# Performance work log

Hardware: AMD Instinct MI355X
Metric: run time of the kernel (lower is better)

Reference implementation:

```python
import jax, jax.numpy as jnp
import numpy as np

N = 100000       # nodes
E = 1600000      # edges (avg degree 16)
F_IN = 64        # node feature dim
H = 8            # GAT heads
C1 = 8           # gat1 out_channels per head (8*8=64)
C2 = 10          # gat2 out_channels = num classes
S = 32           # edge_feats sequence length
SMAX = 32        # s_max padding target
DM = 6           # transformer d_model (SelfAttention dim_out default)
NH = 2           # transformer heads
DIN = 10         # transformer dim_in
NEG = 0.2        # leaky relu negative slope
EPS = 1e-5       # LayerNorm eps


def setup_inputs() -> dict:
    key = jax.random.key(0)
    ks = jax.random.split(key, 32)
    rn = lambda k, shp, s=0.1: jax.random.normal(k, shp, jnp.float32) * s
    inp = {
        'x': jax.random.normal(ks[0], (N, F_IN), jnp.float32),
        'edge_index': jax.random.randint(ks[1], (2, E), 0, N, jnp.int32),
        'edge_feats': jax.random.normal(ks[2], (N, S, DIN), jnp.float32),
        # gat1: weight [in, heads*out], att [1, H, 2*C1], bias [H*C1]
        'W1': rn(ks[3], (F_IN, H * C1)), 'att1': rn(ks[4], (1, H, 2 * C1)), 'b1': jnp.zeros((H * C1,), jnp.float32),
        # gat2: in=70 (64 gat1 + 6 transformer), concat=False -> bias [C2]
        'W2': rn(ks[5], (70, H * C2)), 'att2': rn(ks[6], (1, H, 2 * C2)), 'b2': jnp.zeros((C2,), jnp.float32),
        # transformer Encoder (weights stored [in, out])
        'Wq': rn(ks[7], (DIN, DM)), 'bq': rn(ks[8], (DM,)),
        'Wk': rn(ks[9], (DIN, DM)), 'bk': rn(ks[10], (DM,)),
        'Wv': rn(ks[11], (DIN, DM)), 'bv': rn(ks[12], (DM,)),
        'g0': jnp.ones((DM,), jnp.float32), 'be0': jnp.zeros((DM,), jnp.float32),
        'Wf1': rn(ks[13], (DM, 4 * DM)), 'bf1': rn(ks[14], (4 * DM,)),
        'Wf2': rn(ks[15], (4 * DM, DM)), 'bf2': rn(ks[16], (DM,)),
        'g1': jnp.ones((DM,), jnp.float32), 'be1': jnp.zeros((DM,), jnp.float32),
        'Wrep': rn(ks[17], (SMAX, 1)), 'brep': rn(ks[18], (1,)),
    }
    return inp


def _layer_norm(x, g, b):
    m = x.mean(-1, keepdims=True)
    v = ((x - m) ** 2).mean(-1, keepdims=True)
    return (x - m) / jnp.sqrt(v + EPS) * g + b


def _gat_conv(x, src, dst, W, att, bias, heads, outc, concat):
    """GATConv: remove self loops (masking), add one self loop per node,
    edge-wise attention, per-destination segment softmax, scatter-add."""
    n = x.shape[0]
    valid = src != dst                       # remove_self_loops (mask, static shape)
    loop = jnp.arange(n, dtype=src.dtype)    # add_self_loops
    s = jnp.concatenate([src, loop])
    d = jnp.concatenate([dst, loop])
    valid = jnp.concatenate([valid, jnp.ones((n,), bool)])
    xw = (x @ W).reshape(n, heads, outc)     # [N, H, C]
    xj = xw[s]                               # gather source feats  [E', H, C]
    xi = xw[d]                               # gather target feats  [E', H, C]
    a_i, a_j = att[0, :, :outc], att[0, :, outc:]
    alpha = (xi * a_i).sum(-1) + (xj * a_j).sum(-1)          # [E', H]
    alpha = jnp.where(alpha >= 0, alpha, NEG * alpha)         # leaky relu
    alpha = jnp.where(valid[:, None], alpha, -jnp.inf)        # drop input self-loops
    amax = jax.ops.segment_max(alpha, d, num_segments=n)      # segment softmax
    ea = jnp.exp(alpha - amax[d])
    denom = jax.ops.segment_sum(ea, d, num_segments=n)
    w = ea / denom[d]
    out = jax.ops.segment_sum(xj * w[:, :, None], d, num_segments=n)  # [N, H, C]
    if concat:
        return out.reshape(n, heads * outc) + bias
    return out.mean(axis=1) + bias


def _encoder(Xf, Wq, bq, Wk, bk, Wv, bv, g0, be0, Wf1, bf1, Wf2, bf2, g1, be1, Wrep, brep):
    n, s, _ = Xf.shape
    Q = Xf @ Wq + bq
    K = Xf @ Wk + bk
    V = Xf @ Wv + bv
    dh = DM // NH
    Qh = Q.reshape(n, s, NH, dh).transpose(0, 2, 1, 3)   # [n, h, s, dh]
    Kh = K.reshape(n, s, NH, dh).transpose(0, 2, 1, 3)
    Vh = V.reshape(n, s, NH, dh).transpose(0, 2, 1, 3)
    scale = 1.0 / np.float32(np.sqrt(DM))                # note: sqrt(d_model), as in source
    A = jax.nn.softmax(jnp.einsum('nhsd,nhtd->nhst', Qh, Kh) * scale, axis=-1)
    A1 = jnp.einsum('nhst,nhtd->nhsd', A, Vh)
    O = (Qh + A1).transpose(0, 2, 1, 3).reshape(n, s, DM)  # skip=True path
    O = _layer_norm(O, g0, be0)
    ff = jnp.maximum(O @ Wf1 + bf1, 0.0) @ Wf2 + bf2
    O = _layer_norm(O + ff, g1, be1)
    O = O.transpose(0, 2, 1)                              # [n, DM, s]
    O = jnp.pad(O, ((0, 0), (0, 0), (0, SMAX - s)))
    O = O @ Wrep + brep                                   # fc_rep: [n, DM, 1]
    return O[..., 0]                                      # squeeze -> [n, DM]


def reference(x, edge_index, edge_feats, W1, att1, b1, W2, att2, b2,
              Wq, bq, Wk, bk, Wv, bv, g0, be0, Wf1, bf1, Wf2, bf2,
              g1, be1, Wrep, brep):
    src, dst = edge_index[0], edge_index[1]
    h1 = _gat_conv(x, src, dst, W1, att1, b1, H, C1, True)          # [N, 64]
    h1 = jax.nn.elu(h1)
    xt = _encoder(edge_feats, Wq, bq, Wk, bk, Wv, bv, g0, be0,
                  Wf1, bf1, Wf2, bf2, g1, be1, Wrep, brep)          # [N, 6]
    h2 = _gat_conv(jnp.concatenate([h1, xt], axis=1), src, dst,
                   W2, att2, b2, H, C2, False)                      # [N, 10]
    return jax.nn.log_softmax(h2, axis=1)
```

## Files before the change

kernel.cpp:

```cpp
#include <hip/hip_runtime.h>
#include <hip/hip_bf16.h>


#define NEG_SLOPE 0.2f

using short8  = __attribute__((ext_vector_type(8))) short;
using floatx4 = __attribute__((ext_vector_type(4))) float;

__device__ __forceinline__ float bf_lo(unsigned u) { return __uint_as_float(u << 16); }
__device__ __forceinline__ float bf_hi(unsigned u) { return __uint_as_float(u & 0xffff0000u); }
__device__ __forceinline__ unsigned pk(float lo, float hi)
{
    __hip_bfloat16 l = __float2bfloat16(lo), h = __float2bfloat16(hi);
    unsigned ul = reinterpret_cast<unsigned short&>(l);
    unsigned uh = reinterpret_cast<unsigned short&>(h);
    return ul | (uh << 16);
}
__device__ __forceinline__ short bfs(float f)
{
    __hip_bfloat16 b = __float2bfloat16(f);
    return reinterpret_cast<short&>(b);
}

__global__ void __launch_bounds__(256) front_kernel(
    const float* __restrict__ Xf,
    const float* __restrict__ Wq, const float* __restrict__ bq,
    const float* __restrict__ Wk, const float* __restrict__ bk,
    const float* __restrict__ Wv, const float* __restrict__ bv,
    const float* __restrict__ g0, const float* __restrict__ be0,
    const float* __restrict__ Wf1, const float* __restrict__ bf1,
    const float* __restrict__ Wf2, const float* __restrict__ bf2,
    const float* __restrict__ g1, const float* __restrict__ be1,
    const float* __restrict__ Wrep, const float* __restrict__ brep,
    __hip_bfloat16* __restrict__ hx,
    const int* __restrict__ src, const int* __restrict__ dst,
    int* __restrict__ deg, int* __restrict__ rank, int e,
    int n, int EB)
{
    __shared__ float smem[3072];
    int t = threadIdx.x;
    int bid = blockIdx.x;

    if (bid < EB) {
        float* sh = smem;
        size_t base = (size_t)bid * 2560;
#pragma unroll
        for (int i = 0; i < 10; ++i) sh[i * 256 + t] = Xf[base + i * 256 + t];
        __syncthreads();

        int sub = t >> 5;
        int s   = t & 31;
        int v   = bid * 8 + sub;

        float xv[10];
#pragma unroll
        for (int i = 0; i < 10; ++i) xv[i] = sh[sub * 320 + s * 10 + i];
        __syncthreads();

        float q[6], k[6], w[6];
#pragma unroll
        for (int j = 0; j < 6; ++j) { q[j] = bq[j]; k[j] = bk[j]; w[j] = bv[j]; }
#pragma unroll
        for (int i = 0; i < 10; ++i) {
#pragma unroll
            for (int j = 0; j < 6; ++j) {
                q[j] += xv[i] * Wq[i * 6 + j];
                k[j] += xv[i] * Wk[i * 6 + j];
                w[j] += xv[i] * Wv[i * 6 + j];
            }
        }

        float* kv = sh + sub * 384;
        *(float4*)&kv[s * 12 + 0] = make_float4(k[0], k[1], k[2], k[3]);
        *(float4*)&kv[s * 12 + 4] = make_float4(k[4], k[5], w[0], w[1]);
        *(float4*)&kv[s * 12 + 8] = make_float4(w[2], w[3], w[4], w[5]);
        __builtin_amdgcn_wave_barrier();

        const float scale = 0.40824829046386301637f;
        float q0s = q[0] * scale, q1s = q[1] * scale, q2s = q[2] * scale;
        float q3s = q[3] * scale, q4s = q[4] * scale, q5s = q[5] * scale;

        float dA0 = 0.f, dB0 = 0.f, dA1 = 0.f, dB1 = 0.f;
        float aA00 = 0.f, aA01 = 0.f, aA02 = 0.f;
        float aB00 = 0.f, aB01 = 0.f, aB02 = 0.f;
        float aA10 = 0.f, aA11 = 0.f, aA12 = 0.f;
        float aB10 = 0.f, aB11 = 0.f, aB12 = 0.f;

#pragma unroll 4
        for (int t2 = 0; t2 < 32; t2 += 2) {
            float4 A0 = *(const float4*)&kv[t2 * 12 + 0];
            float4 A1 = *(const float4*)&kv[t2 * 12 + 4];
            float4 A2 = *(const float4*)&kv[t2 * 12 + 8];
            float4 B0 = *(const float4*)&kv[t2 * 12 + 12];
            float4 B1 = *(const float4*)&kv[t2 * 12 + 16];
            float4 B2 = *(const float4*)&kv[t2 * 12 + 20];
            {
                float p0 = __expf(q0s * A0.x + q1s * A0.y + q2s * A0.z);
                float p1 = __expf(q3s * A0.w + q4s * A1.x + q5s * A1.y);
                dA0 += p0; aA00 += p0 * A1.z; aA01 += p0 * A1.w; aA02 += p0 * A2.x;
                dA1 += p1; aA10 += p1 * A2.y; aA11 += p1 * A2.z; aA12 += p1 * A2.w;
            }
            {
                float p0 = __expf(q0s * B0.x + q1s * B0.y + q2s * B0.z);
                float p1 = __expf(q3s * B0.w + q4s * B1.x + q5s * B1.y);
                dB0 += p0; aB00 += p0 * B1.z; aB01 += p0 * B1.w; aB02 += p0 * B2.x;
                dB1 += p1; aB10 += p1 * B2.y; aB11 += p1 * B2.z; aB12 += p1 * B2.w;
            }
        }

        float O[6];
        {
            float inv0 = 1.f / (dA0 + dB0);
            float inv1 = 1.f / (dA1 + dB1);
            O[0] = q[0] + (aA00 + aB00) * inv0;
            O[1] = q[1] + (aA01 + aB01) * inv0;
            O[2] = q[2] + (aA02 + aB02) * inv0;
            O[3] = q[3] + (aA10 + aB10) * inv1;
            O[4] = q[4] + (aA11 + aB11) * inv1;
            O[5] = q[5] + (aA12 + aB12) * inv1;
        }

        {
            float mean = (O[0] + O[1] + O[2] + O[3] + O[4] + O[5]) * (1.f / 6.f);
            float var = 0.f;
#pragma unroll
            for (int j = 0; j < 6; ++j) { float d = O[j] - mean; var += d * d; }
            var *= (1.f / 6.f);
            float r = rsqrtf(var + 1e-5f);
#pragma unroll
            for (int j = 0; j < 6; ++j) O[j] = (O[j] - mean) * r * g0[j] + be0[j];
        }

        float f[6];
#pragma unroll
        for (int j = 0; j < 6; ++j) f[j] = O[j] + bf2[j];
#pragma unroll 4
        for (int r = 0; r < 24; ++r) {
            float hr = bf1[r];
#pragma unroll
            for (int j = 0; j < 6; ++j) hr += O[j] * Wf1[j * 24 + r];
            hr = fmaxf(hr, 0.f);
#pragma unroll
            for (int j = 0; j < 6; ++j) f[j] += hr * Wf2[r * 6 + j];
        }
        {
            float mean = (f[0] + f[1] + f[2] + f[3] + f[4] + f[5]) * (1.f / 6.f);
            float var = 0.f;
#pragma unroll
            for (int j = 0; j < 6; ++j) { float d = f[j] - mean; var += d * d; }
            var *= (1.f / 6.f);
            float r = rsqrtf(var + 1e-5f);
#pragma unroll
            for (int j = 0; j < 6; ++j) f[j] = (f[j] - mean) * r * g1[j] + be1[j];
        }

        float wr = Wrep[s];
#pragma unroll
        for (int j = 0; j < 6; ++j) {
            float val = f[j] * wr;
#pragma unroll
            for (int off = 16; off >= 1; off >>= 1) val += __shfl_xor(val, off, 32);
            f[j] = val;
        }
        if (s == 0) {
            float br = brep[0];
#pragma unroll
            for (int j = 0; j < 6; ++j)
                hx[(size_t)v * 96 + 64 + j] = __float2bfloat16(f[j] + br);
        }
    } else {
        int i = (bid - EB) * 256 + t;
        if (i < e) {
            int ss = src[i], dd = dst[i];
            if (ss != dd) rank[i] = atomicAdd(&deg[dd], 1);
        }
    }
}

__global__ void __launch_bounds__(256) w1ext_kernel(
    const float* __restrict__ W1, const float* __restrict__ att1,
    __hip_bfloat16* __restrict__ w1t)
{
    int idx = blockIdx.x * 256 + threadIdx.x;
    if (idx >= 80 * 64) return;
    int j = idx / 64, k = idx % 64;
    float val;
    if (j < 64) {
        val = W1[k * 64 + j];
    } else if (j < 72) {
        int h = j - 64;
        val = 0.f;
        for (int c = 0; c < 8; ++c)
            val += W1[k * 64 + h * 8 + c] * att1[h * 16 + c];
    } else {
        int h = j - 72;
        val = 0.f;
        for (int c = 0; c < 8; ++c)
            val += W1[k * 64 + h * 8 + c] * att1[h * 16 + 8 + c];
    }
    w1t[j * 64 + k] = __float2bfloat16(val);
}

__global__ void __launch_bounds__(256) xw1mfma_kernel(
    const float* __restrict__ x, const __hip_bfloat16* __restrict__ w1t,
    __hip_bfloat16* __restrict__ xwb, float* __restrict__ ai,
    unsigned* __restrict__ ajp, int n)
{
    int t = threadIdx.x, wv = t >> 6, l = t & 63;
    int base = blockIdx.x * 64 + wv * 16;
    if (base >= n) return;

    int mrow = l & 15;
    int kc   = (l >> 4) * 8;
    int dr0  = (l >> 4) * 4;

    const float* xr = x + (size_t)(base + mrow) * 64;
    short8 a0, a1;
#pragma unroll
    for (int i = 0; i < 8; ++i) {
        a0[i] = bfs(xr[kc + i]);
        a1[i] = bfs(xr[32 + kc + i]);
    }

    const short* wp = (const short*)w1t;

#pragma unroll
    for (int nt = 0; nt < 5; ++nt) {
        int col = nt * 16 + mrow;
        short8 b0 = *(const short8*)(wp + (size_t)col * 64 + kc);
        short8 b1 = *(const short8*)(wp + (size_t)col * 64 + 32 + kc);
        floatx4 acc = {0.f, 0.f, 0.f, 0.f};
        acc = __builtin_amdgcn_mfma_f32_16x16x32_bf16(a0, b0, acc, 0, 0, 0);
        acc = __builtin_amdgcn_mfma_f32_16x16x32_bf16(a1, b1, acc, 0, 0, 0);
        if (nt < 4) {
#pragma unroll
            for (int r = 0; r < 4; ++r) {
                int m = base + dr0 + r;
                xwb[(size_t)m * 64 + nt * 16 + mrow] = __float2bfloat16(acc[r]);
            }
        } else {
#pragma unroll
            for (int r = 0; r < 4; ++r) {
                int m = base + dr0 + r;
                float val = acc[r];
                float nb  = __shfl_xor(val, 1, 64);
                if (mrow < 8) {
                    ai[(size_t)m * 8 + mrow] = val;
                } else {
                    int h = mrow - 8;
                    if ((h & 1) == 0)
                        ajp[(size_t)m * 4 + (h >> 1)] = pk(val, nb);
                }
            }
        }
    }
}

__global__ void __launch_bounds__(1024) scan1_kernel(
    const int* __restrict__ deg, int* __restrict__ bsum, int n)
{
    __shared__ int sh[1024];
    int t = threadIdx.x;
    int i = blockIdx.x * 1024 + t;
    sh[t] = (i < n) ? deg[i] : 0;
    __syncthreads();
    for (int off = 512; off >= 1; off >>= 1) {
        if (t < off) sh[t] += sh[t + off];
        __syncthreads();
    }
    if (t == 0) bsum[blockIdx.x] = sh[0];
}

__global__ void __launch_bounds__(128) scan2_kernel(int* __restrict__ bsum, int nb)
{
    __shared__ int sh[128];
    int t = threadIdx.x;
    int v = (t < nb) ? bsum[t] : 0;
    sh[t] = v;
    __syncthreads();
    for (int off = 1; off < 128; off <<= 1) {
        int val = (t >= off) ? sh[t - off] : 0;
        __syncthreads();
        sh[t] += val;
        __syncthreads();
    }
    if (t < nb) bsum[t] = sh[t] - v;
}

__global__ void __launch_bounds__(1024) scan3_kernel(
    const int* __restrict__ deg, const int* __restrict__ bsum,
    int* __restrict__ offs, int n)
{
    __shared__ int sh[1024];
    int t = threadIdx.x;
    int i = blockIdx.x * 1024 + t;
    int v = (i < n) ? deg[i] : 0;
    sh[t] = v;
    __syncthreads();
    for (int off = 1; off < 1024; off <<= 1) {
        int val = (t >= off) ? sh[t - off] : 0;
        __syncthreads();
        sh[t] += val;
        __syncthreads();
    }
    if (i < n) offs[i] = bsum[blockIdx.x] + sh[t] - v;
}

__global__ void scatter_kernel(const int* __restrict__ src, const int* __restrict__ dst,
                               const int* __restrict__ offsets,
                               const int* __restrict__ rank,
                               int* __restrict__ elist, int e)
{
    int i = blockIdx.x * blockDim.x + threadIdx.x;
    if (i < e) {
        int s = src[i], d = dst[i];
        if (s != d) elist[offsets[d] + rank[i]] = s;
    }
}

__global__ void __launch_bounds__(256) agg1_kernel(
    const __hip_bfloat16* __restrict__ xwb, const float* __restrict__ ai1,
    const unsigned* __restrict__ ajp, const float* __restrict__ att1,
    const float* __restrict__ b1,
    const int* __restrict__ offs, const int* __restrict__ deg,
    const int* __restrict__ elist,
    __hip_bfloat16* __restrict__ hx, int n)
{
    int t = threadIdx.x, wv = t >> 6, l = t & 63;
    int v = blockIdx.x * 4 + wv;
    int h = l >> 3, c = l & 7;
    int e1 = l >> 3, hp = l & 7;

    float ai_l = ai1[(size_t)v * 8 + h];
    float ai_p = ai1[(size_t)v * 8 + hp];
    float attj_l = att1[h * 16 + 8 + c];

    float yself = __bfloat162float(xwb[(size_t)v * 64 + l]);
    float ps = yself * attj_l;
    ps += __shfl_xor(ps, 1, 64);
    ps += __shfl_xor(ps, 2, 64);
    ps += __shfl_xor(ps, 4, 64);
    float a = ai_l + ps;
    a = fmaxf(a, NEG_SLOPE * a);
    float ea  = __expf(a);
    float acc = ea * yself;

    float den_acc = 0.f;
    int off = offs[v], dg = deg[v];
    for (int j = 0; j < dg; j += 8) {
        int idxv = 0;
        if (l < 8 && j + l < dg) idxv = elist[off + j + l];
        int se = __shfl(idxv, e1, 64);
        unsigned aw = ajp[(size_t)se * 4 + (hp >> 1)];
        float ajv = (hp & 1) ? bf_hi(aw) : bf_lo(aw);
        float u = ai_p + ajv;
        u = fmaxf(u, NEG_SLOPE * u);
        float wl = __expf(u);
        wl = (j + e1 < dg) ? wl : 0.f;
        den_acc += wl;
#pragma unroll
        for (int b = 0; b < 8; ++b) {
            int s = __shfl(idxv, b, 64);
            float y = __bfloat162float(xwb[(size_t)s * 64 + l]);
            float w = __shfl(wl, b * 8 + h, 64);
            acc += w * y;
        }
    }
    den_acc += __shfl_xor(den_acc, 8, 64);
    den_acc += __shfl_xor(den_acc, 16, 64);
    den_acc += __shfl_xor(den_acc, 32, 64);
    float den = ea + __shfl(den_acc, h, 64);

    float o = acc / den + b1[l];
    o = o > 0.f ? o : expm1f(o);
    hx[(size_t)v * 96 + l] = __float2bfloat16(o);
}

__global__ void __launch_bounds__(256) w2ext_kernel(
    const float* __restrict__ W2, const float* __restrict__ att2,
    __hip_bfloat16* __restrict__ w2t)
{
    int idx = blockIdx.x * 256 + threadIdx.x;
    if (idx >= 96 * 96) return;
    int j = idx / 96, k = idx % 96;
    float val = 0.f;
    if (k < 70) {
        if (j < 80) {
            val = W2[k * 80 + j];
        } else if (j < 88) {
            int h = j - 80;
            for (int c = 0; c < 10; ++c)
                val += W2[k * 80 + h * 10 + c] * att2[h * 20 + c];
        } else {
            int h = j - 88;
            for (int c = 0; c < 10; ++c)
                val += W2[k * 80 + h * 10 + c] * att2[h * 20 + 10 + c];
        }
    }
    w2t[j * 96 + k] = __float2bfloat16(val);
}

__global__ void __launch_bounds__(256) xw2mfma_kernel(
    const __hip_bfloat16* __restrict__ hx, const __hip_bfloat16* __restrict__ w2t,
    __hip_bfloat16* __restrict__ xw2p, float* __restrict__ ai2, int n)
{
    int t = threadIdx.x, wv = t >> 6, l = t & 63;
    int base = blockIdx.x * 64 + wv * 16;
    if (base >= n) return;

    int mrow = l & 15;
    int kc   = (l >> 4) * 8;
    int dr0  = (l >> 4) * 4;

    const short* hp = (const short*)hx;
    const short* wp = (const short*)w2t;

    short8 a0 = *(const short8*)(hp + (size_t)(base + mrow) * 96 + 0  + kc);
    short8 a1 = *(const short8*)(hp + (size_t)(base + mrow) * 96 + 32 + kc);
    short8 a2 = *(const short8*)(hp + (size_t)(base + mrow) * 96 + 64 + kc);

#pragma unroll
    for (int nt = 0; nt < 6; ++nt) {
        int col = nt * 16 + mrow;
        short8 b0 = *(const short8*)(wp + (size_t)col * 96 + 0  + kc);
        short8 b1 = *(const short8*)(wp + (size_t)col * 96 + 32 + kc);
        short8 b2 = *(const short8*)(wp + (size_t)col * 96 + 64 + kc);
        floatx4 acc = {0.f, 0.f, 0.f, 0.f};
        acc = __builtin_amdgcn_mfma_f32_16x16x32_bf16(a0, b0, acc, 0, 0, 0);
        acc = __builtin_amdgcn_mfma_f32_16x16x32_bf16(a1, b1, acc, 0, 0, 0);
        acc = __builtin_amdgcn_mfma_f32_16x16x32_bf16(a2, b2, acc, 0, 0, 0);
#pragma unroll
        for (int r = 0; r < 4; ++r) {
            int m = base + dr0 + r;
            float val = acc[r];
            if (nt < 5) {
                xw2p[(size_t)m * 128 + nt * 16 + mrow] = __float2bfloat16(val);
            } else {
                if (mrow < 8) ai2[(size_t)m * 8 + mrow] = val;
                else xw2p[(size_t)m * 128 + 80 + (mrow - 8)] = __float2bfloat16(val);
            }
        }
    }
}

__global__ void __launch_bounds__(256) agg2_kernel(
    const unsigned* __restrict__ xw2p, const float* __restrict__ ai2,
    const float* __restrict__ b2,
    const int* __restrict__ offs, const int* __restrict__ deg,
    const int* __restrict__ elist, float* __restrict__ out, int n)
{
    __shared__ float buf[4][80];
    __shared__ float buf2[4][10];
    int t = threadIdx.x, wv = t >> 6, l = t & 63;
    int v = blockIdx.x * 4 + wv;

    int hc = (l < 40) ? (l / 5) : 0;
    int e1 = l >> 3, hp = l & 7;
    float ai_p = ai2[(size_t)v * 8 + hp];
    float ai_l = (l < 40) ? ai2[(size_t)v * 8 + hc] : 0.f;

    bool act = l < 44;
    unsigned selfw = act ? xw2p[(size_t)v * 64 + l] : 0u;
    int ajl = 40 + (hc >> 1);
    unsigned ajw = __shfl(selfw, ajl, 64);
    float ajs = (hc & 1) ? bf_hi(ajw) : bf_lo(ajw);
    float a = ai_l + ajs;
    a = fmaxf(a, NEG_SLOPE * a);
    float e0 = __expf(a);
    float acc0 = e0 * bf_lo(selfw), acc1 = e0 * bf_hi(selfw);

    float den_acc = 0.f;
    int off = offs[v], dg = deg[v];
    for (int j = 0; j < dg; j += 8) {
        int idxv = 0;
        if (l < 8 && j + l < dg) idxv = elist[off + j + l];
        int se = __shfl(idxv, e1, 64);
        unsigned aw = xw2p[(size_t)se * 64 + 40 + (hp >> 1)];
        float ajv = (hp & 1) ? bf_hi(aw) : bf_lo(aw);
        float u = ai_p + ajv;
        u = fmaxf(u, NEG_SLOPE * u);
        float wl = __expf(u);
        wl = (j + e1 < dg) ? wl : 0.f;
        den_acc += wl;
#pragma unroll
        for (int b = 0; b < 8; ++b) {
            int s = __shfl(idxv, b, 64);
            unsigned yw = (l < 40) ? xw2p[(size_t)s * 64 + l] : 0u;
            float w = __shfl(wl, b * 8 + hc, 64);
            acc0 += w * bf_lo(yw);
            acc1 += w * bf_hi(yw);
        }
    }
    den_acc += __shfl_xor(den_acc, 8, 64);
    den_acc += __shfl_xor(den_acc, 16, 64);
    den_acc += __shfl_xor(den_acc, 32, 64);
    float den = e0 + __shfl(den_acc, hc, 64);

    if (l < 40) {
        float inv = 1.f / den;
        buf[wv][2 * l]     = acc0 * inv;
        buf[wv][2 * l + 1] = acc1 * inv;
    }
    __builtin_amdgcn_wave_barrier();
    if (l < 10) {
        float mval = 0.f;
#pragma unroll
        for (int hh = 0; hh < 8; ++hh) mval += buf[wv][hh * 10 + l];
        buf2[wv][l] = mval * 0.125f + b2[l];
    }
    __builtin_amdgcn_wave_barrier();
    if (l < 10) {
        float mx = -1e30f;
#pragma unroll
        for (int cc = 0; cc < 10; ++cc) mx = fmaxf(mx, buf2[wv][cc]);
        float se = 0.f;
#pragma unroll
        for (int cc = 0; cc < 10; ++cc) se += __expf(buf2[wv][cc] - mx);
        out[(size_t)v * 10 + l] = buf2[wv][l] - mx - __logf(se);
    }
}

extern "C" void kernel_launch(void* const* d_in, const int* in_sizes, int n_in,
                              void* d_out, int out_size, void* d_ws, size_t ws_size,
                              hipStream_t stream)
{
    const float* x    = (const float*)d_in[0];
    const int*   ei   = (const int*)  d_in[1];
    const float* ef   = (const float*)d_in[2];
    const float* W1   = (const float*)d_in[3];
    const float* att1 = (const float*)d_in[4];
    const float* b1   = (const float*)d_in[5];
    const float* W2   = (const float*)d_in[6];
    const float* att2 = (const float*)d_in[7];
    const float* b2   = (const float*)d_in[8];
    const float* Wq   = (const float*)d_in[9];
    const float* bq   = (const float*)d_in[10];
    const float* Wk   = (const float*)d_in[11];
    const float* bk   = (const float*)d_in[12];
    const float* Wv   = (const float*)d_in[13];
    const float* bv   = (const float*)d_in[14];
    const float* g0   = (const float*)d_in[15];
    const float* be0  = (const float*)d_in[16];
    const float* Wf1  = (const float*)d_in[17];
    const float* bf1  = (const float*)d_in[18];
    const float* Wf2  = (const float*)d_in[19];
    const float* bf2  = (const float*)d_in[20];
    const float* g1   = (const float*)d_in[21];
    const float* be1  = (const float*)d_in[22];
    const float* Wrep = (const float*)d_in[23];
    const float* brep = (const float*)d_in[24];

    const int n = in_sizes[0] / 64;
    const int e = in_sizes[1] / 2;
    const int* src = ei;
    const int* dst = ei + e;

    char* ws = (char*)d_ws;
    size_t o = 0;
    auto alloc = [&](size_t bytes) -> void* {
        void* p = ws + o;
        o += (bytes + 255) & ~(size_t)255;
        return p;
    };
    __hip_bfloat16* xw1b = (__hip_bfloat16*)alloc((size_t)n * 64 * 2);
    __hip_bfloat16* hx   = (__hip_bfloat16*)alloc((size_t)n * 96 * 2);
    __hip_bfloat16* xw2p = (__hip_bfloat16*)alloc((size_t)n * 128 * 2);
    __hip_bfloat16* w2t  = (__hip_bfloat16*)alloc(96 * 96 * 2);
    __hip_bfloat16* w1t  = (__hip_bfloat16*)alloc(80 * 64 * 2);
    unsigned* ajp = (unsigned*)alloc((size_t)n * 4 * 4);
    float* ai1   = (float*)alloc((size_t)n * 8 * 4);
    float* ai2   = (float*)alloc((size_t)n * 8 * 4);
    int*   deg   = (int*)  alloc((size_t)n * 4);
    int*   offs  = (int*)  alloc((size_t)n * 4);
    int*   rank  = (int*)  alloc((size_t)e * 4);
    int*   bsum  = (int*)  alloc(256 * 4);
    int*   elist = (int*)  alloc((size_t)e * 4);
    (void)ws_size; (void)n_in; (void)out_size;

    hipMemsetAsync(deg, 0, (size_t)n * 4, stream);
    hipMemsetAsync(hx, 0, (size_t)n * 96 * 2, stream);

    const int NB = (n + 1023) / 1024;
    const int EB = n / 8;
    const int CB = (e + 255) / 256;

    w2ext_kernel<<<36, 256, 0, stream>>>(W2, att2, w2t);
    w1ext_kernel<<<20, 256, 0, stream>>>(W1, att1, w1t);
    front_kernel<<<EB + CB, 256, 0, stream>>>(
        ef, Wq, bq, Wk, bk, Wv, bv, g0, be0, Wf1, bf1, Wf2, bf2, g1, be1,
        Wrep, brep, hx,
        src, dst, deg, rank, e,
        n, EB);
    xw1mfma_kernel<<<(n + 63) / 64, 256, 0, stream>>>(x, w1t, xw1b, ai1, ajp, n);
    scan1_kernel<<<NB, 1024, 0, stream>>>(deg, bsum, n);
    scan2_kernel<<<1, 128, 0, stream>>>(bsum, NB);
    scan3_kernel<<<NB, 1024, 0, stream>>>(deg, bsum, offs, n);
    scatter_kernel<<<(e + 255) / 256, 256, 0, stream>>>(src, dst, offs, rank,
                                                        elist, e);
    agg1_kernel<<<n / 4, 256, 0, stream>>>(xw1b, ai1, ajp, att1, b1,
                                           offs, deg, elist, hx, n);
    xw2mfma_kernel<<<(n + 63) / 64, 256, 0, stream>>>(hx, w2t, xw2p, ai2, n);
    agg2_kernel<<<n / 4, 256, 0, stream>>>((const unsigned*)xw2p, ai2, b2,
                                           offs, deg, elist, (float*)d_out, n);
}
```

Before: 380.7 us.

## Merge weight prep and deg zeroing, fold xw1 MFMA into front kernel

Replaces the two memsets and both weight-extension kernels with a single prep kernel that also zeroes the degree array. The x·W1 MFMA projection becomes an extra block range inside the front kernel, so it runs alongside the transformer encoder and the degree-counting atomics. The full memset of hx is dropped; agg1 now zeroes the padding columns 70–95 of each row itself. This cuts launch count and memset traffic, at the cost of a larger heterogeneous grid whose block types may not balance well.

```diff
diff --git a/kernel.cpp b/kernel.cpp
--- a/kernel.cpp
+++ b/kernel.cpp
@@ -20,6 +20,53 @@
 {
     __hip_bfloat16 b = __float2bfloat16(f);
     return reinterpret_cast<short&>(b);
+}
+
+__global__ void __launch_bounds__(256) prep_kernel(
+    const float* __restrict__ W1, const float* __restrict__ att1,
+    __hip_bfloat16* __restrict__ w1t,
+    const float* __restrict__ W2, const float* __restrict__ att2,
+    __hip_bfloat16* __restrict__ w2t,
+    int* __restrict__ deg, int n)
+{
+    int i = blockIdx.x * 256 + threadIdx.x;
+    if (i < n) deg[i] = 0;
+    if (i < 80 * 64) {
+        int j = i / 64, k = i % 64;
+        float val;
+        if (j < 64) {
+            val = W1[k * 64 + j];
+        } else if (j < 72) {
+            int h = j - 64;
+            val = 0.f;
+            for (int c = 0; c < 8; ++c)
+                val += W1[k * 64 + h * 8 + c] * att1[h * 16 + c];
+        } else {
+            int h = j - 72;
+            val = 0.f;
+            for (int c = 0; c < 8; ++c)
+                val += W1[k * 64 + h * 8 + c] * att1[h * 16 + 8 + c];
+        }
+        w1t[j * 64 + k] = __float2bfloat16(val);
+    }
+    if (i < 96 * 96) {
+        int j = i / 96, k = i % 96;
+        float val = 0.f;
+        if (k < 70) {
+            if (j < 80) {
+                val = W2[k * 80 + j];
+            } else if (j < 88) {
+                int h = j - 80;
+                for (int c = 0; c < 10; ++c)
+                    val += W2[k * 80 + h * 10 + c] * att2[h * 20 + c];
+            } else {
+                int h = j - 88;
+                for (int c = 0; c < 10; ++c)
+                    val += W2[k * 80 + h * 10 + c] * att2[h * 20 + 10 + c];
+            }
+        }
+        w2t[j * 96 + k] = __float2bfloat16(val);
+    }
 }
 
 __global__ void __launch_bounds__(256) front_kernel(
@@ -35,7 +82,10 @@
     __hip_bfloat16* __restrict__ hx,
     const int* __restrict__ src, const int* __restrict__ dst,
     int* __restrict__ deg, int* __restrict__ rank, int e,
-    int n, int EB)
+    const float* __restrict__ x, const __hip_bfloat16* __restrict__ w1t,
+    __hip_bfloat16* __restrict__ xwb, float* __restrict__ ai,
+    unsigned* __restrict__ ajp,
+    int n, int EB, int CB)
 {
     __shared__ float smem[3072];
     int t = threadIdx.x;
@@ -168,88 +218,60 @@
             for (int j = 0; j < 6; ++j)
                 hx[(size_t)v * 96 + 64 + j] = __float2bfloat16(f[j] + br);
         }
-    } else {
+    } else if (bid < EB + CB) {
         int i = (bid - EB) * 256 + t;
         if (i < e) {
             int ss = src[i], dd = dst[i];
             if (ss != dd) rank[i] = atomicAdd(&deg[dd], 1);
         }
-    }
-}
-
-__global__ void __launch_bounds__(256) w1ext_kernel(
-    const float* __restrict__ W1, const float* __restrict__ att1,
-    __hip_bfloat16* __restrict__ w1t)
-{
-    int idx = blockIdx.x * 256 + threadIdx.x;
-    if (idx >= 80 * 64) return;
-    int j = idx / 64, k = idx % 64;
-    float val;
-    if (j < 64) {
-        val = W1[k * 64 + j];
-    } else if (j < 72) {
-        int h = j - 64;
-        val = 0.f;
-        for (int c = 0; c < 8; ++c)
-            val += W1[k * 64 + h * 8 + c] * att1[h * 16 + c];
     } else {
-        int h = j - 72;
-        val = 0.f;
-        for (int c = 0; c < 8; ++c)
-            val += W1[k * 64 + h * 8 + c] * att1[h * 16 + 8 + c];
-    }
-    w1t[j * 64 + k] = __float2bfloat16(val);
-}
-
-__global__ void __launch_bounds__(256) xw1mfma_kernel(
-    const float* __restrict__ x, const __hip_bfloat16* __restrict__ w1t,
-    __hip_bfloat16* __restrict__ xwb, float* __restrict__ ai,
-    unsigned* __restrict__ ajp, int n)
-{
-    int t = threadIdx.x, wv = t >> 6, l = t & 63;
-    int base = blockIdx.x * 64 + wv * 16;
-    if (base >= n) return;
-
-    int mrow = l & 15;
-    int kc   = (l >> 4) * 8;
-    int dr0  = (l >> 4) * 4;
-
-    const float* xr = x + (size_t)(base + mrow) * 64;
-    short8 a0, a1;
-#pragma unroll
-    for (int i = 0; i < 8; ++i) {
-        a0[i] = bfs(xr[kc + i]);
-        a1[i] = bfs(xr[32 + kc + i]);
-    }
-
-    const short* wp = (const short*)w1t;
-
-#pragma unroll
-    for (int nt = 0; nt < 5; ++nt) {
-        int col = nt * 16 + mrow;
-        short8 b0 = *(const short8*)(wp + (size_t)col * 64 + kc);
-        short8 b1 = *(const short8*)(wp + (size_t)col * 64 + 32 + kc);
-        floatx4 acc = {0.f, 0.f, 0.f, 0.f};
-        acc = __builtin_amdgcn_mfma_f32_16x16x32_bf16(a0, b0, acc, 0, 0, 0);
-        acc = __builtin_amdgcn_mfma_f32_16x16x32_bf16(a1, b1, acc, 0, 0, 0);
-        if (nt < 4) {
-#pragma unroll
-            for (int r = 0; r < 4; ++r) {
-                int m = base + dr0 + r;
-                xwb[(size_t)m * 64 + nt * 16 + mrow] = __float2bfloat16(acc[r]);
+        int xb = bid - EB - CB;
+        int wv = t >> 6, l = t & 63;
+        int base = xb * 64 + wv * 16;
+        if (base < n) {
+            int mrow = l & 15;
+            int kc   = (l >> 4) * 8;
+            int dr0  = (l >> 4) * 4;
+
+            const float* xr = x + (size_t)(base + mrow) * 64;
+            short8 a0, a1;
+#pragma unroll
+            for (int i = 0; i < 8; ++i) {
+                a0[i] = bfs(xr[kc + i]);
+                a1[i] = bfs(xr[32 + kc + i]);
             }
-        } else {
-#pragma unroll
-            for (int r = 0; r < 4; ++r) {
-                int m = base + dr0 + r;
-                float val = acc[r];
-                float nb  = __shfl_xor(val, 1, 64);
-                if (mrow < 8) {
-                    ai[(size_t)m * 8 + mrow] = val;
+
+            const short* wp = (const short*)w1t;
+
+#pragma unroll
+            for (int nt = 0; nt < 5; ++nt) {
+                int col = nt * 16 + mrow;
+                short8 b0 = *(const short8*)(wp + (size_t)col * 64 + kc);
+                short8 b1 = *(const short8*)(wp + (size_t)col * 64 + 32 + kc);
+                floatx4 acc = {0.f, 0.f, 0.f, 0.f};
+                acc = __builtin_amdgcn_mfma_f32_16x16x32_bf16(a0, b0, acc, 0, 0, 0);
+                acc = __builtin_amdgcn_mfma_f32_16x16x32_bf16(a1, b1, acc, 0, 0, 0);
+                if (nt < 4) {
+#pragma unroll
+                    for (int r = 0; r < 4; ++r) {
+                        int m = base + dr0 + r;
+                        xwb[(size_t)m * 64 + nt * 16 + mrow] =
+                            __float2bfloat16(acc[r]);
+                    }
                 } else {
-                    int h = mrow - 8;
-                    if ((h & 1) == 0)
-                        ajp[(size_t)m * 4 + (h >> 1)] = pk(val, nb);
+#pragma unroll
+                    for (int r = 0; r < 4; ++r) {
+                        int m = base + dr0 + r;
+                        float val = acc[r];
+                        float nb  = __shfl_xor(val, 1, 64);
+                        if (mrow < 8) {
+                            ai[(size_t)m * 8 + mrow] = val;
+                        } else {
+                            int h = mrow - 8;
+                            if ((h & 1) == 0)
+                                ajp[(size_t)m * 4 + (h >> 1)] = pk(val, nb);
+                        }
+                    }
                 }
             }
         }
@@ -374,30 +396,8 @@
     float o = acc / den + b1[l];
     o = o > 0.f ? o : expm1f(o);
     hx[(size_t)v * 96 + l] = __float2bfloat16(o);
-}
-
-__global__ void __launch_bounds__(256) w2ext_kernel(
-    const float* __restrict__ W2, const float* __restrict__ att2,
-    __hip_bfloat16* __restrict__ w2t)
-{
-    int idx = blockIdx.x * 256 + threadIdx.x;
-    if (idx >= 96 * 96) return;
-    int j = idx / 96, k = idx % 96;
-    float val = 0.f;
-    if (k < 70) {
-        if (j < 80) {
-            val = W2[k * 80 + j];
-        } else if (j < 88) {
-            int h = j - 80;
-            for (int c = 0; c < 10; ++c)
-                val += W2[k * 80 + h * 10 + c] * att2[h * 20 + c];
-        } else {
-            int h = j - 88;
-            for (int c = 0; c < 10; ++c)
-                val += W2[k * 80 + h * 10 + c] * att2[h * 20 + 10 + c];
-        }
-    }
-    w2t[j * 96 + k] = __float2bfloat16(val);
+    unsigned* rowu = (unsigned*)(hx + (size_t)v * 96);
+    if (l < 13) rowu[35 + l] = 0u;
 }
 
 __global__ void __launch_bounds__(256) xw2mfma_kernel(
@@ -577,21 +577,19 @@
     int*   elist = (int*)  alloc((size_t)e * 4);
     (void)ws_size; (void)n_in; (void)out_size;
 
-    hipMemsetAsync(deg, 0, (size_t)n * 4, stream);
-    hipMemsetAsync(hx, 0, (size_t)n * 96 * 2, stream);
-
     const int NB = (n + 1023) / 1024;
     const int EB = n / 8;
     const int CB = (e + 255) / 256;
-
-    w2ext_kernel<<<36, 256, 0, stream>>>(W2, att2, w2t);
-    w1ext_kernel<<<20, 256, 0, stream>>>(W1, att1, w1t);
-    front_kernel<<<EB + CB, 256, 0, stream>>>(
+    const int XB = (n + 63) / 64;
+
+    prep_kernel<<<(n + 255) / 256, 256, 0, stream>>>(W1, att1, w1t,
+                                                     W2, att2, w2t, deg, n);
+    front_kernel<<<EB + CB + XB, 256, 0, stream>>>(
         ef, Wq, bq, Wk, bk, Wv, bv, g0, be0, Wf1, bf1, Wf2, bf2, g1, be1,
         Wrep, brep, hx,
         src, dst, deg, rank, e,
-        n, EB);
-    xw1mfma_kernel<<<(n + 63) / 64, 256, 0, stream>>>(x, w1t, xw1b, ai1, ajp, n);
+        x, w1t, xw1b, ai1, ajp,
+        n, EB, CB);
     scan1_kernel<<<NB, 1024, 0, stream>>>(deg, bsum, n);
     scan2_kernel<<<1, 128, 0, stream>>>(bsum, NB);
     scan3_kernel<<<NB, 1024, 0, stream>>>(deg, bsum, offs, n);
```

Result: no change. 373.9 us (-1.8%).
